# Performance work log

Measured on AMD Instinct MI355X. Metric: run time of the kernel, lower is better.

The kernel has to match this reference:

```python
import jax, jax.numpy as jnp
import numpy as np

DIM = 1024
H = 16
D = DIM // H
CS = 64  # chunk_size
SCALE = D ** -0.5


def setup_inputs() -> dict:
    key = jax.random.key(0)
    k1, k2, k3 = jax.random.split(key, 3)
    B, N = 4, 4096
    x = jax.random.normal(k1, (B, N, DIM), dtype=jnp.float32)
    # torch nn.Linear(dim, 3*dim, bias=False): y = x @ W.T, W:[3*dim, dim].
    # We store the transposed layout W_qkv:[dim, 3*dim] so y = x @ W_qkv.
    W_qkv = jax.random.normal(k2, (DIM, 3 * DIM), dtype=jnp.float32) * (DIM ** -0.5)
    W_out = jax.random.normal(k3, (DIM, DIM), dtype=jnp.float32) * (DIM ** -0.5)
    return {"x": x, "W_qkv": W_qkv, "W_out": W_out}


def reference(x, W_qkv, W_out):
    B, N, C = x.shape
    qkv = (x @ W_qkv).reshape(B, N, 3, H, D)
    qkv = jnp.transpose(qkv, (2, 0, 3, 1, 4))  # [3,B,H,N,D]
    q, k, v = qkv[0], qkv[1], qkv[2]
    # N chosen divisible by CS, so no padding needed (pad=0 branch).
    nc = N // CS
    q = q.reshape(B, H, nc, CS, D)
    k = k.reshape(B, H, nc, CS, D)
    v = v.reshape(B, H, nc, CS, D)
    # Local quadratic attention within each chunk, causal mask.
    attn = jnp.einsum('bhcqd,bhckd->bhcqk', q, k) * SCALE
    mask = jnp.triu(jnp.ones((CS, CS), dtype=bool), k=1)
    attn = jnp.where(mask, jnp.float32(-65000.0), attn)
    attn = jax.nn.softmax(attn, axis=-1)
    out_local = jnp.einsum('bhcqk,bhckd->bhcqd', attn, v)
    # Cross-chunk linear term (num_chunks > 1): mean-pooled K/V, exclusive cumsum.
    chunk_k = k.mean(axis=3)  # [B,H,nc,D]
    chunk_v = v.mean(axis=3)
    cum_k = jnp.cumsum(chunk_k, axis=2)
    cum_v = jnp.cumsum(chunk_v, axis=2)
    zeros = jnp.zeros((B, H, 1, D), dtype=x.dtype)
    cum_k = jnp.concatenate([zeros, cum_k[:, :, :-1]], axis=2)
    cum_v = jnp.concatenate([zeros, cum_v[:, :, :-1]], axis=2)
    cross = jax.nn.sigmoid(jnp.einsum('bhcsd,bhcd->bhcs', q, cum_k) * SCALE)
    out = out_local + cross[..., None] * cum_v[:, :, :, None, :] * 0.5
    out = out.reshape(B, H, N, D)
    out = jnp.transpose(out, (0, 2, 1, 3)).reshape(B, N, C)
    return out @ W_out
```

## Files before the change

### kernel.cpp

```cpp
#include <hip/hip_runtime.h>
#include <stdint.h>

typedef __attribute__((ext_vector_type(4))) float f32x4;
typedef __attribute__((ext_vector_type(8))) short short8;
typedef unsigned short u16;

#define NH 16
#define HD 64
#define SEQ 4096
#define BATCH 4
#define NROWS (BATCH * SEQ)
#define DIMC 1024
#define QKVC 3072
#define SCALE 0.125f

__device__ __forceinline__ u16 f2bf(float f) {
  union { float f; uint32_t u; } v; v.f = f;
  uint32_t u = v.u;
  uint32_t r = (u + 0x7fffu + ((u >> 16) & 1u)) >> 16;
  return (u16)r;
}
__device__ __forceinline__ float bf2f(u16 h) {
  union { uint32_t u; float f; } v; v.u = ((uint32_t)h) << 16;
  return v.f;
}

__global__ __launch_bounds__(256) void cvt_kernel(const float* __restrict__ in,
                                                  u16* __restrict__ out, int n4) {
  int i = blockIdx.x * 256 + threadIdx.x;
  if (i >= n4) return;
  float4 v = ((const float4*)in)[i];
  ushort4 o;
  o.x = f2bf(v.x); o.y = f2bf(v.y); o.z = f2bf(v.z); o.w = f2bf(v.w);
  ((ushort4*)out)[i] = o;
}

__global__ __launch_bounds__(256) void transpose_cvt(const float* __restrict__ in,
                                                     u16* __restrict__ out, int R, int C) {
  __shared__ float t[32][33];
  int nbx = C >> 5;
  int bx = blockIdx.x % nbx, by = blockIdx.x / nbx;
  int r0 = by << 5, c0 = bx << 5;
  int tid = threadIdx.x;
#pragma unroll
  for (int i = 0; i < 4; i++) {
    int id = i * 256 + tid; int lr = id >> 5, lc = id & 31;
    t[lr][lc] = in[(size_t)(r0 + lr) * C + (c0 + lc)];
  }
  __syncthreads();
#pragma unroll
  for (int i = 0; i < 4; i++) {
    int id = i * 256 + tid; int lr = id >> 5, lc = id & 31;
    out[(size_t)(c0 + lr) * R + (r0 + lc)] = f2bf(t[lc][lr]);
  }
}

template <int OUT_BF16>
__global__ __launch_bounds__(512, 2) void gemm_bt(const u16* __restrict__ A,
                                                  const u16* __restrict__ Bt,
                                                  void* __restrict__ Cv,
                                                  int M, int N, int K) {
  __shared__ __align__(16) u16 lds2[2][32768];
  int nbx = N >> 8;
  int nwg = gridDim.x;
  int bid = blockIdx.x;
  int cpx = nwg >> 3;
  int swz = (bid & 7) * cpx + (bid >> 3);
  int bx = swz % nbx, by = swz / nbx;
  int tid = threadIdx.x, lane = tid & 63, wv = tid >> 6;
  int wr = wv >> 2, wc = wv & 3;
  int lr = lane & 15, g = lane >> 4;
  int rx = lr & 7;
  int rsub = lane >> 3;
  int clog = (lane & 7) ^ rsub;

  const u16* Ap = A + (size_t)(by * 256) * K;
  const u16* Bp = Bt + (size_t)(bx * 256) * K;

  f32x4 acc[8][4];
#pragma unroll
  for (int m = 0; m < 8; m++)
#pragma unroll
    for (int n = 0; n < 4; n++) acc[m][n] = (f32x4){0.f, 0.f, 0.f, 0.f};

  short8 a0[4][2], a1[4][2], b0[2][2], b1[2][2];

#define ISSUE_A(HALF, L, T) do {                                                \
    int ru_ = (HALF) * 128 + (L) * 64 + wv * 8;                                 \
    const u16* g_ = Ap + (size_t)(ru_ + rsub) * K + (T) * 64 + clog * 8;        \
    __builtin_amdgcn_global_load_lds(                                           \
        (const __attribute__((address_space(1))) uint32_t*)g_,                  \
        (__attribute__((address_space(3))) uint32_t*)&lds2[(T) & 1][ru_ * 64],  \
        16, 0, 0);                                                              \
  } while (0)

#define ISSUE_B(HALF, L, T) do {                                                \
    int ru_ = (HALF) * 128 + (L) * 64 + wv * 8;                                 \
    const u16* g_ = Bp + (size_t)(ru_ + rsub) * K + (T) * 64 + clog * 8;        \
    __builtin_amdgcn_global_load_lds(                                           \
        (const __attribute__((address_space(1))) uint32_t*)g_,                  \
        (__attribute__((address_space(3)))                                      \
             uint32_t*)&lds2[(T) & 1][16384 + ru_ * 64],                        \
        16, 0, 0);                                                              \
  } while (0)

#define LDA(DST, MH, T) do {                                                    \
    _Pragma("unroll")                                                           \
    for (int m2 = 0; m2 < 4; m2++) {                                            \
      int row_ = wr * 128 + ((MH) * 4 + m2) * 16 + lr;                          \
      const u16* bp_ = &lds2[(T) & 1][row_ * 64];                               \
      _Pragma("unroll")                                                         \
      for (int s = 0; s < 2; s++)                                               \
        DST[m2][s] = *(const short8*)(bp_ + (((s * 4 + g) ^ rx) << 3));         \
    }                                                                           \
  } while (0)

#define LDB(DST, NHh, T) do {                                                   \
    _Pragma("unroll")                                                           \
    for (int n2 = 0; n2 < 2; n2++) {                                            \
      int row_ = wc * 64 + ((NHh) * 2 + n2) * 16 + lr;                          \
      const u16* bp_ = &lds2[(T) & 1][16384 + row_ * 64];                       \
      _Pragma("unroll")                                                         \
      for (int s = 0; s < 2; s++)                                               \
        DST[n2][s] = *(const short8*)(bp_ + (((s * 4 + g) ^ rx) << 3));         \
    }                                                                           \
  } while (0)

#define MFMA_Q(MH, NHh, AA, BB) do {                                            \
    _Pragma("unroll")                                                           \
    for (int s = 0; s < 2; s++)                                                 \
      _Pragma("unroll")                                                         \
      for (int m2 = 0; m2 < 4; m2++)                                            \
        _Pragma("unroll")                                                       \
        for (int n2 = 0; n2 < 2; n2++)                                          \
          acc[(MH) * 4 + m2][(NHh) * 2 + n2] =                                  \
              __builtin_amdgcn_mfma_f32_16x16x32_bf16(                          \
                  AA[m2][s], BB[n2][s], acc[(MH) * 4 + m2][(NHh) * 2 + n2],     \
                  0, 0, 0);                                                     \
  } while (0)

  int NT = K >> 6;
  ISSUE_A(0, 0, 0); ISSUE_A(0, 1, 0);
  ISSUE_B(0, 0, 0); ISSUE_B(0, 1, 0);
  ISSUE_B(1, 0, 0); ISSUE_B(1, 1, 0);
  ISSUE_A(1, 0, 0); ISSUE_A(1, 1, 0);
  ISSUE_A(0, 0, 1); ISSUE_A(0, 1, 1);
  ISSUE_B(0, 0, 1); ISSUE_B(0, 1, 1);
  ISSUE_B(1, 0, 1); ISSUE_B(1, 1, 1);
  __builtin_amdgcn_sched_barrier(0);
  asm volatile("s_waitcnt vmcnt(6)" ::: "memory");
  __builtin_amdgcn_sched_barrier(0);
  __builtin_amdgcn_s_barrier();

  for (int t = 0; t < NT; t++) {
    LDA(a0, 0, t);
    LDB(b0, 0, t);
    if (t + 1 < NT) { ISSUE_A(1, 0, t + 1); ISSUE_A(1, 1, t + 1); }
    __builtin_amdgcn_s_barrier();
    asm volatile("s_waitcnt lgkmcnt(0)" ::: "memory");
    __builtin_amdgcn_sched_barrier(0);
    __builtin_amdgcn_s_setprio(1);
    MFMA_Q(0, 0, a0, b0);
    __builtin_amdgcn_s_setprio(0);
    __builtin_amdgcn_s_barrier();
    LDB(b1, 1, t);
    __builtin_amdgcn_s_barrier();
    asm volatile("s_waitcnt lgkmcnt(0)" ::: "memory");
    __builtin_amdgcn_sched_barrier(0);
    __builtin_amdgcn_s_setprio(1);
    MFMA_Q(0, 1, a0, b1);
    __builtin_amdgcn_s_setprio(0);
    __builtin_amdgcn_s_barrier();
    LDA(a1, 1, t);
    if (t + 2 < NT) { ISSUE_B(0, 0, t + 2); ISSUE_B(0, 1, t + 2); }
    __builtin_amdgcn_s_barrier();
    asm volatile("s_waitcnt lgkmcnt(0)" ::: "memory");
    __builtin_amdgcn_sched_barrier(0);
    __builtin_amdgcn_s_setprio(1);
    MFMA_Q(1, 1, a1, b1);
    __builtin_amdgcn_s_setprio(0);
    __builtin_amdgcn_s_barrier();
    if (t + 2 < NT) {
      ISSUE_B(1, 0, t + 2); ISSUE_B(1, 1, t + 2);
      ISSUE_A(0, 0, t + 2); ISSUE_A(0, 1, t + 2);
    }
    __builtin_amdgcn_sched_barrier(0);
    if (t < NT - 2)
      asm volatile("s_waitcnt vmcnt(6)" ::: "memory");
    else
      asm volatile("s_waitcnt vmcnt(0)" ::: "memory");
    __builtin_amdgcn_sched_barrier(0);
    __builtin_amdgcn_s_barrier();
    __builtin_amdgcn_s_setprio(1);
    MFMA_Q(1, 0, a1, b0);
    __builtin_amdgcn_s_setprio(0);
  }

#undef ISSUE_A
#undef ISSUE_B
#undef LDA
#undef LDB
#undef MFMA_Q

  int rb = by * 256 + wr * 128, cb = bx * 256 + wc * 64;
#pragma unroll
  for (int m = 0; m < 8; m++)
#pragma unroll
    for (int n = 0; n < 4; n++)
#pragma unroll
      for (int r = 0; r < 4; r++) {
        int rg = rb + m * 16 + g * 4 + r;
        int cg = cb + n * 16 + lr;
        float v = acc[m][n][r];
        if (OUT_BF16)
          ((u16*)Cv)[(size_t)rg * N + cg] = f2bf(v);
        else
          ((float*)Cv)[(size_t)rg * N + cg] = v;
      }
}

__global__ void chunk_sums(const u16* __restrict__ qkv, float* __restrict__ ck,
                           float* __restrict__ cv) {
  int blk = blockIdx.x;
  int c = blk & 63, h = (blk >> 6) & 15, b = blk >> 10;
  int d = threadIdx.x;
  const u16* base = qkv + (size_t)(b * SEQ + c * 64) * QKVC + 1024 + h * 64 + d;
  float sk = 0.f, sv = 0.f;
  for (int r = 0; r < 64; r++) {
    sk += bf2f(base[(size_t)r * QKVC]);
    sv += bf2f(base[(size_t)r * QKVC + 1024]);
  }
  ck[(size_t)blk * 64 + d] = sk * 0.015625f;
  cv[(size_t)blk * 64 + d] = sv * 0.015625f;
}

__global__ void cumsum_excl(const float* __restrict__ ck, const float* __restrict__ cv,
                            float* __restrict__ cuk, float* __restrict__ cuv) {
  int bh = blockIdx.x;
  int d = threadIdx.x;
  float ak = 0.f, av = 0.f;
  for (int c = 0; c < 64; c++) {
    size_t i = ((size_t)bh * 64 + c) * 64 + d;
    cuk[i] = ak; cuv[i] = av;
    ak += ck[i]; av += cv[i];
  }
}

__global__ __launch_bounds__(256) void attn_kernel(const u16* __restrict__ qkv,
                                                   const float* __restrict__ cuk,
                                                   const float* __restrict__ cuv,
                                                   u16* __restrict__ out) {
  int blk = blockIdx.x;
  int c = blk & 63, h = (blk >> 6) & 15, b = blk >> 10;
  int row0 = b * SEQ + c * 64;
  __shared__ u16 q_s[64][80];
  __shared__ u16 k_s[64][80];
  __shared__ u16 vt_s[64][80];
  __shared__ u16 p_s[64][80];
  __shared__ u16 ck_s[64];
  __shared__ float cv_s[64];
  int tid = threadIdx.x;
  {
    int r = tid >> 2, qt = tid & 3;
    const u16* rp = qkv + (size_t)(row0 + r) * QKVC + h * 64 + qt * 16;
    uint4 q0 = *(const uint4*)rp;          uint4 q1 = *(const uint4*)(rp + 8);
    uint4 k0 = *(const uint4*)(rp + 1024); uint4 k1 = *(const uint4*)(rp + 1032);
    uint4 v0 = *(const uint4*)(rp + 2048); uint4 v1 = *(const uint4*)(rp + 2056);
    *(uint4*)&q_s[r][qt * 16] = q0;     *(uint4*)&q_s[r][qt * 16 + 8] = q1;
    *(uint4*)&k_s[r][qt * 16] = k0;     *(uint4*)&k_s[r][qt * 16 + 8] = k1;
    const u16* vv0 = (const u16*)&v0;   const u16* vv1 = (const u16*)&v1;
#pragma unroll
    for (int j = 0; j < 8; j++) vt_s[qt * 16 + j][r] = vv0[j];
#pragma unroll
    for (int j = 0; j < 8; j++) vt_s[qt * 16 + 8 + j][r] = vv1[j];
    if (tid < 64) {
      ck_s[tid] = f2bf(cuk[(size_t)blk * 64 + tid]);
      cv_s[tid] = cuv[(size_t)blk * 64 + tid];
    }
  }
  __syncthreads();

  int lane = tid & 63, w = tid >> 6;
  int lr = lane & 15, g = lane >> 4;
  f32x4 accS[4];
#pragma unroll
  for (int n = 0; n < 4; n++) accS[n] = (f32x4){0.f, 0.f, 0.f, 0.f};
  f32x4 accC = (f32x4){0.f, 0.f, 0.f, 0.f};
  short8 zf = (short8){0, 0, 0, 0, 0, 0, 0, 0};
#pragma unroll
  for (int kt = 0; kt < 2; kt++) {
    int lk = kt * 32 + g * 8;
    short8 af = *(const short8*)&q_s[w * 16 + lr][lk];
    short8 cf = (lr == 0) ? *(const short8*)&ck_s[lk] : zf;
    accC = __builtin_amdgcn_mfma_f32_16x16x32_bf16(af, cf, accC, 0, 0, 0);
#pragma unroll
    for (int n = 0; n < 4; n++) {
      short8 bf = *(const short8*)&k_s[n * 16 + lr][lk];
      accS[n] = __builtin_amdgcn_mfma_f32_16x16x32_bf16(af, bf, accS[n], 0, 0, 0);
    }
  }
  float crossv[4];
#pragma unroll
  for (int r4 = 0; r4 < 4; r4++) {
    int row = w * 16 + g * 4 + r4;
    float x[4];
    float mx = -3.4e38f;
#pragma unroll
    for (int n = 0; n < 4; n++) {
      int col = n * 16 + lr;
      x[n] = ((col & 63) > (row & 63)) ? -65000.0f : accS[n][r4] * SCALE;
      mx = fmaxf(mx, x[n]);
    }
    mx = fmaxf(mx, __shfl_xor(mx, 1));
    mx = fmaxf(mx, __shfl_xor(mx, 2));
    mx = fmaxf(mx, __shfl_xor(mx, 4));
    mx = fmaxf(mx, __shfl_xor(mx, 8));
    float p[4], sum = 0.f;
#pragma unroll
    for (int n = 0; n < 4; n++) { p[n] = __expf(x[n] - mx); sum += p[n]; }
    sum += __shfl_xor(sum, 1);
    sum += __shfl_xor(sum, 2);
    sum += __shfl_xor(sum, 4);
    sum += __shfl_xor(sum, 8);
    float inv = 1.0f / sum;
#pragma unroll
    for (int n = 0; n < 4; n++) p_s[row][n * 16 + lr] = f2bf(p[n] * inv);
    float sg = 1.0f / (1.0f + __expf(-accC[r4] * SCALE));
    crossv[r4] = __shfl(sg, (lane & 48));
  }
  __syncthreads();
  f32x4 accO[4];
#pragma unroll
  for (int n = 0; n < 4; n++) accO[n] = (f32x4){0.f, 0.f, 0.f, 0.f};
#pragma unroll
  for (int kt = 0; kt < 2; kt++) {
    int lk = kt * 32 + g * 8;
    short8 pf = *(const short8*)&p_s[w * 16 + lr][lk];
#pragma unroll
    for (int n = 0; n < 4; n++) {
      short8 vf = *(const short8*)&vt_s[n * 16 + lr][lk];
      accO[n] = __builtin_amdgcn_mfma_f32_16x16x32_bf16(pf, vf, accO[n], 0, 0, 0);
    }
  }
#pragma unroll
  for (int n = 0; n < 4; n++)
#pragma unroll
    for (int r4 = 0; r4 < 4; r4++) {
      int row = w * 16 + g * 4 + r4;
      int col = n * 16 + lr;
      float v = accO[n][r4] + crossv[r4] * cv_s[col] * 0.5f;
      out[(size_t)(row0 + row) * DIMC + h * 64 + col] = f2bf(v);
    }
}

extern "C" void kernel_launch(void* const* d_in, const int* in_sizes, int n_in,
                              void* d_out, int out_size, void* d_ws, size_t ws_size,
                              hipStream_t stream) {
  const float* x = (const float*)d_in[0];
  const float* Wqkv = (const float*)d_in[1];
  const float* Wout = (const float*)d_in[2];
  char* ws = (char*)d_ws;
  size_t off = 0;
  auto alloc = [&](size_t b) {
    void* p = ws + off;
    off += (b + 255) & ~(size_t)255;
    return p;
  };
  u16* xb = (u16*)alloc((size_t)NROWS * DIMC * 2);
  u16* wqt = (u16*)alloc((size_t)QKVC * DIMC * 2);
  u16* wot = (u16*)alloc((size_t)DIMC * DIMC * 2);
  u16* qkvb = (u16*)alloc((size_t)NROWS * QKVC * 2);
  float* chk = (float*)alloc((size_t)4096 * 64 * 4);
  float* chv = (float*)alloc((size_t)4096 * 64 * 4);
  float* cuk = (float*)alloc((size_t)4096 * 64 * 4);
  float* cuv = (float*)alloc((size_t)4096 * 64 * 4);
  u16* attnb = xb;

  cvt_kernel<<<16384, 256, 0, stream>>>(x, xb, NROWS * DIMC / 4);
  transpose_cvt<<<3072, 256, 0, stream>>>(Wqkv, wqt, DIMC, QKVC);
  transpose_cvt<<<1024, 256, 0, stream>>>(Wout, wot, DIMC, DIMC);
  gemm_bt<1><<<768, 512, 0, stream>>>(xb, wqt, qkvb, NROWS, QKVC, DIMC);
  chunk_sums<<<4096, 64, 0, stream>>>(qkvb, chk, chv);
  cumsum_excl<<<64, 64, 0, stream>>>(chk, chv, cuk, cuv);
  attn_kernel<<<4096, 256, 0, stream>>>(qkvb, cuk, cuv, attnb);
  gemm_bt<0><<<256, 512, 0, stream>>>(attnb, wot, d_out, NROWS, DIMC, DIMC);
}
```

Measured before the change: 215.4 us.

## Simplify GEMM pipeline to one-tile prefetch and vectorize chunk sums

The GEMM main loop's hand-tuned two-stage prefetch, with its many barriers and explicit vmcnt waits, is replaced by a simpler schedule. Each iteration reads all LDS fragments, issues global loads for the next tile, runs the four MFMA quadrants back to back, and ends with one __syncthreads. This cuts barrier overhead but exposes more global-load latency, since only one tile is in flight and the barrier drains outstanding loads. Separately, chunk_sums now uses 256 blocks of 256 threads that read four bf16 columns at once across all heads, replacing 4096 blocks of 64 threads doing scalar loads.

Measured after the change: 214.1 us. No clear change (-0.6%).

```diff
diff --git a/kernel.cpp b/kernel.cpp
--- a/kernel.cpp
+++ b/kernel.cpp
@@ -140,60 +140,37 @@
   } while (0)
 
   int NT = K >> 6;
-  ISSUE_A(0, 0, 0); ISSUE_A(0, 1, 0);
-  ISSUE_B(0, 0, 0); ISSUE_B(0, 1, 0);
-  ISSUE_B(1, 0, 0); ISSUE_B(1, 1, 0);
-  ISSUE_A(1, 0, 0); ISSUE_A(1, 1, 0);
-  ISSUE_A(0, 0, 1); ISSUE_A(0, 1, 1);
-  ISSUE_B(0, 0, 1); ISSUE_B(0, 1, 1);
-  ISSUE_B(1, 0, 1); ISSUE_B(1, 1, 1);
-  __builtin_amdgcn_sched_barrier(0);
-  asm volatile("s_waitcnt vmcnt(6)" ::: "memory");
-  __builtin_amdgcn_sched_barrier(0);
-  __builtin_amdgcn_s_barrier();
+  ISSUE_A(0, 0, 0); ISSUE_A(0, 1, 0); ISSUE_A(1, 0, 0); ISSUE_A(1, 1, 0);
+  ISSUE_B(0, 0, 0); ISSUE_B(0, 1, 0); ISSUE_B(1, 0, 0); ISSUE_B(1, 1, 0);
+  __syncthreads();
 
   for (int t = 0; t < NT; t++) {
     LDA(a0, 0, t);
     LDB(b0, 0, t);
-    if (t + 1 < NT) { ISSUE_A(1, 0, t + 1); ISSUE_A(1, 1, t + 1); }
-    __builtin_amdgcn_s_barrier();
-    asm volatile("s_waitcnt lgkmcnt(0)" ::: "memory");
+    __builtin_amdgcn_sched_barrier(0);
+    if (t + 1 < NT) {
+      ISSUE_A(0, 0, t + 1); ISSUE_A(0, 1, t + 1);
+      ISSUE_A(1, 0, t + 1); ISSUE_A(1, 1, t + 1);
+    }
+    __builtin_amdgcn_sched_barrier(0);
+    LDB(b1, 1, t);
+    LDA(a1, 1, t);
+    __builtin_amdgcn_sched_barrier(0);
+    if (t + 1 < NT) {
+      ISSUE_B(0, 0, t + 1); ISSUE_B(0, 1, t + 1);
+      ISSUE_B(1, 0, t + 1); ISSUE_B(1, 1, t + 1);
+    }
     __builtin_amdgcn_sched_barrier(0);
     __builtin_amdgcn_s_setprio(1);
     MFMA_Q(0, 0, a0, b0);
-    __builtin_amdgcn_s_setprio(0);
-    __builtin_amdgcn_s_barrier();
-    LDB(b1, 1, t);
-    __builtin_amdgcn_s_barrier();
-    asm volatile("s_waitcnt lgkmcnt(0)" ::: "memory");
-    __builtin_amdgcn_sched_barrier(0);
-    __builtin_amdgcn_s_setprio(1);
+    __builtin_amdgcn_sched_barrier(0);
     MFMA_Q(0, 1, a0, b1);
-    __builtin_amdgcn_s_setprio(0);
-    __builtin_amdgcn_s_barrier();
-    LDA(a1, 1, t);
-    if (t + 2 < NT) { ISSUE_B(0, 0, t + 2); ISSUE_B(0, 1, t + 2); }
-    __builtin_amdgcn_s_barrier();
-    asm volatile("s_waitcnt lgkmcnt(0)" ::: "memory");
-    __builtin_amdgcn_sched_barrier(0);
-    __builtin_amdgcn_s_setprio(1);
+    __builtin_amdgcn_sched_barrier(0);
     MFMA_Q(1, 1, a1, b1);
-    __builtin_amdgcn_s_setprio(0);
-    __builtin_amdgcn_s_barrier();
-    if (t + 2 < NT) {
-      ISSUE_B(1, 0, t + 2); ISSUE_B(1, 1, t + 2);
-      ISSUE_A(0, 0, t + 2); ISSUE_A(0, 1, t + 2);
-    }
-    __builtin_amdgcn_sched_barrier(0);
-    if (t < NT - 2)
-      asm volatile("s_waitcnt vmcnt(6)" ::: "memory");
-    else
-      asm volatile("s_waitcnt vmcnt(0)" ::: "memory");
-    __builtin_amdgcn_sched_barrier(0);
-    __builtin_amdgcn_s_barrier();
-    __builtin_amdgcn_s_setprio(1);
+    __builtin_amdgcn_sched_barrier(0);
     MFMA_Q(1, 0, a1, b0);
     __builtin_amdgcn_s_setprio(0);
+    __syncthreads();
   }
 
 #undef ISSUE_A
@@ -219,19 +196,27 @@
       }
 }
 
-__global__ void chunk_sums(const u16* __restrict__ qkv, float* __restrict__ ck,
-                           float* __restrict__ cv) {
-  int blk = blockIdx.x;
-  int c = blk & 63, h = (blk >> 6) & 15, b = blk >> 10;
-  int d = threadIdx.x;
-  const u16* base = qkv + (size_t)(b * SEQ + c * 64) * QKVC + 1024 + h * 64 + d;
-  float sk = 0.f, sv = 0.f;
+__global__ __launch_bounds__(256) void chunk_sums(const u16* __restrict__ qkv,
+                                                  float* __restrict__ ck,
+                                                  float* __restrict__ cv) {
+  int b = blockIdx.x >> 6, c = blockIdx.x & 63;
+  int col = threadIdx.x * 4;
+  const u16* base = qkv + (size_t)(b * SEQ + c * 64) * QKVC + 1024 + col;
+  float sk0 = 0.f, sk1 = 0.f, sk2 = 0.f, sk3 = 0.f;
+  float sv0 = 0.f, sv1 = 0.f, sv2 = 0.f, sv3 = 0.f;
+#pragma unroll 8
   for (int r = 0; r < 64; r++) {
-    sk += bf2f(base[(size_t)r * QKVC]);
-    sv += bf2f(base[(size_t)r * QKVC + 1024]);
-  }
-  ck[(size_t)blk * 64 + d] = sk * 0.015625f;
-  cv[(size_t)blk * 64 + d] = sv * 0.015625f;
+    ushort4 kk = *(const ushort4*)(base + (size_t)r * QKVC);
+    ushort4 vv = *(const ushort4*)(base + (size_t)r * QKVC + 1024);
+    sk0 += bf2f(kk.x); sk1 += bf2f(kk.y); sk2 += bf2f(kk.z); sk3 += bf2f(kk.w);
+    sv0 += bf2f(vv.x); sv1 += bf2f(vv.y); sv2 += bf2f(vv.z); sv3 += bf2f(vv.w);
+  }
+  int h = col >> 6, d = col & 63;
+  size_t o = (((size_t)(b * 16 + h)) * 64 + c) * 64 + d;
+  ck[o]     = sk0 * 0.015625f; ck[o + 1] = sk1 * 0.015625f;
+  ck[o + 2] = sk2 * 0.015625f; ck[o + 3] = sk3 * 0.015625f;
+  cv[o]     = sv0 * 0.015625f; cv[o + 1] = sv1 * 0.015625f;
+  cv[o + 2] = sv2 * 0.015625f; cv[o + 3] = sv3 * 0.015625f;
 }
 
 __global__ void cumsum_excl(const float* __restrict__ ck, const float* __restrict__ cv,
@@ -380,7 +365,7 @@
   transpose_cvt<<<3072, 256, 0, stream>>>(Wqkv, wqt, DIMC, QKVC);
   transpose_cvt<<<1024, 256, 0, stream>>>(Wout, wot, DIMC, DIMC);
   gemm_bt<1><<<768, 512, 0, stream>>>(xb, wqt, qkvb, NROWS, QKVC, DIMC);
-  chunk_sums<<<4096, 64, 0, stream>>>(qkvb, chk, chv);
+  chunk_sums<<<256, 256, 0, stream>>>(qkvb, chk, chv);
   cumsum_excl<<<64, 64, 0, stream>>>(chk, chv, cuk, cuv);
   attn_kernel<<<4096, 256, 0, stream>>>(qkvb, cuk, cuv, attnb);
   gemm_bt<0><<<256, 512, 0, stream>>>(attnb, wot, d_out, NROWS, DIMC, DIMC);
```
